# Optimization experiments

Measured on AMD Instinct MI355X. Metric: run time of the kernel, lower is better.

## Reference

```python
import jax, jax.numpy as jnp
import numpy as np

NUM_ROUTES = 32 * 6 * 6  # 1152
NUM_CAPS = 10
IN_DIM = 8
OUT_DIM = 16
NUM_ITERS = 3

def _conv(x, w, stride):
    return jax.lax.conv_general_dilated(
        x, w, window_strides=(stride, stride), padding='VALID',
        dimension_numbers=('NCHW', 'OIHW', 'NCHW'))

def _squash(u):
    # squash over last axis, exactly as torch code (no eps)
    sn = (u ** 2).sum(-1, keepdims=True)
    return sn * u / ((1.0 + sn) * jnp.sqrt(sn))

def setup_inputs() -> dict:
    key = jax.random.key(0)
    ks = jax.random.split(key, 10)
    B = 512
    data = jax.random.normal(ks[0], (B, 1, 28, 28), dtype=jnp.float32)
    conv_w = jax.random.normal(ks[1], (256, 1, 9, 9), dtype=jnp.float32) * 0.05
    conv_b = jnp.zeros((256,), dtype=jnp.float32)
    # 8 primary-capsule convs stacked caps-major -> fused conv [8*32,256,9,9]
    pc_w = jax.random.normal(ks[2], (8 * 32, 256, 9, 9), dtype=jnp.float32) * 0.01
    pc_b = jnp.zeros((8 * 32,), dtype=jnp.float32)
    W = jax.random.normal(ks[3], (NUM_ROUTES, NUM_CAPS, OUT_DIM, IN_DIM), dtype=jnp.float32)
    enc_w1 = jax.random.normal(ks[4], (512, OUT_DIM * NUM_CAPS), dtype=jnp.float32) * 0.05
    enc_b1 = jnp.zeros((512,), dtype=jnp.float32)
    enc_w2 = jax.random.normal(ks[5], (9, 512), dtype=jnp.float32) * 0.05
    enc_b2 = jnp.zeros((9,), dtype=jnp.float32)
    return dict(data=data, conv_w=conv_w, conv_b=conv_b, pc_w=pc_w, pc_b=pc_b,
                W=W, enc_w1=enc_w1, enc_b1=enc_b1, enc_w2=enc_w2, enc_b2=enc_b2)

def reference(data, conv_w, conv_b, pc_w, pc_b, W, enc_w1, enc_b1, enc_w2, enc_b2):
    B = data.shape[0]
    # ConvLayer: conv + relu -> [B,256,20,20]
    x = jax.nn.relu(_conv(data, conv_w, 1) + conv_b[None, :, None, None])
    # PrimaryCaps: 8 stride-2 convs (fused, caps-major channels) -> [B,256,6,6]
    u = _conv(x, pc_w, 2) + pc_b[None, :, None, None]
    # torch: stack(dim=1) then view(B, num_routes, -1) == reshape caps-major flat
    u = u.reshape(B, NUM_ROUTES, IN_DIM)
    u = _squash(u)  # [B,R,8]
    # WaferCaps: u_hat[b,r,c,o] = sum_i W[r,c,o,i] * u[b,r,i]
    u_hat = jnp.einsum('rcoi,bri->brco', W, u)  # [B,R,C,O]
    b_ij = jnp.zeros((NUM_ROUTES, NUM_CAPS), dtype=u_hat.dtype)
    v = None
    for it in range(NUM_ITERS):
        c_ij = jax.nn.softmax(b_ij, axis=0)  # softmax over routes (dim=1 in torch)
        s = jnp.einsum('rc,brco->bco', c_ij, u_hat)  # [B,C,O]
        # original squashes [B,1,C,O,1] over last (size-1) dim -> elementwise
        s2 = s ** 2
        v = s2 * s / ((1.0 + s2) * jnp.sqrt(s2))  # = s*|s|/(1+s^2)
        if it < NUM_ITERS - 1:
            a = jnp.einsum('brco,bco->brc', u_hat, v)  # [B,R,C]
            b_ij = b_ij + a.mean(axis=0)
    # Encoder: flatten [B,C,O] row-major -> [B,160]
    flat = v.reshape(B, NUM_CAPS * OUT_DIM)
    h = jax.nn.relu(flat @ enc_w1.T + enc_b1)  # dropout is identity at eval
    out = jax.nn.sigmoid(h @ enc_w2.T + enc_b2)
    return out
```

## Files before the change

### kernel.cpp

```cpp
#include <hip/hip_runtime.h>
#include <hip/hip_bf16.h>
#include <stdint.h>


typedef __bf16 bf16_t;
typedef __bf16 bf16x4 __attribute__((ext_vector_type(4)));
typedef __bf16 bf16x8 __attribute__((ext_vector_type(8)));
typedef float f32x4 __attribute__((ext_vector_type(4)));
typedef int i32x4 __attribute__((ext_vector_type(4)));
typedef int i32x8 __attribute__((ext_vector_type(8)));

__device__ __forceinline__ void gload_lds16(const void* g, void* l) {
    __builtin_amdgcn_global_load_lds((const __attribute__((address_space(1))) void*)g,
                                     (__attribute__((address_space(3))) void*)l, 16, 0, 0);
}

#define MEMBAR() asm volatile("" ::: "memory")

__device__ __forceinline__ uint8_t fp8b(float v) {
    return (uint8_t)(__builtin_amdgcn_cvt_pk_fp8_f32(v, 0.f, 0, false) & 0xFF);
}

__global__ __launch_bounds__(256) void k_prep(const float* __restrict__ w1,
                                              const float* __restrict__ cw,
                                              const float* __restrict__ pcw,
                                              float* __restrict__ w1t,
                                              bf16_t* __restrict__ Bc1,
                                              float* __restrict__ bij,
                                              uint8_t* __restrict__ w2t8) {
    __shared__ uint16_t tmp16[10368];
    int blk = blockIdx.x, tid = threadIdx.x;
    if (blk < 45) {
        int i = blk * 256 + tid;
        if (i < 11520) bij[i] = 0.f;
    } else if (blk < 365) {
        int i = (blk - 45) * 256 + tid;
        int j = i / 160, k = i % 160;
        w1t[k * 512 + j] = w1[i];
    } else if (blk < 469) {
        int i = (blk - 365) * 256 + tid;
        if (i < 26624) {
            int oc = i / 104, k = i % 104;
            Bc1[i] = (k < 81) ? (bf16_t)cw[oc * 81 + k] : (bf16_t)0.f;
        }
    } else {
        int oc = blk - 469;
        const float* src = pcw + (size_t)oc * 20736;
        for (int q2 = tid; q2 < 10368; q2 += 256) {
            float a = src[q2 * 2] * 64.f;
            float b = src[q2 * 2 + 1] * 64.f;
            uint32_t pk = __builtin_amdgcn_cvt_pk_fp8_f32(a, b, 0, false);
            tmp16[q2] = (uint16_t)(pk & 0xFFFF);
        }
        __syncthreads();
        uint32_t* dst = (uint32_t*)(w2t8 + (size_t)oc * 20736);
        for (int w = tid; w < 5184; w += 256) {
            int k = w * 4;
            int t = k >> 8, ic0 = k & 255;
            uint32_t r = 0;
#pragma unroll
            for (int j = 0; j < 4; ++j) {
                int s = (ic0 + j) * 81 + t;
                uint32_t b = (tmp16[s >> 1] >> ((s & 1) * 8)) & 0xFF;
                r |= b << (8 * j);
            }
            dst[w] = r;
        }
    }
}

__global__ __launch_bounds__(512) void k_c1gemm(const float* __restrict__ data,
                                                const bf16_t* __restrict__ Bc1,
                                                const float* __restrict__ cb,
                                                uint8_t* __restrict__ xt8) {
    __shared__ __align__(16) bf16_t As[128 * 104];
    __shared__ __align__(16) bf16_t Bs[256 * 104];
    int tid = threadIdx.x, lane = tid & 63, wave = tid >> 6;
    int wm = wave >> 2, wn = wave & 3;
    for (int i = tid; i < 3328; i += 512) {
        int byte = i * 16;
        int r = byte / 208;
        int c16 = (byte - r * 208) >> 4;
        gload_lds16(Bc1 + r * 104 + c16 * 8, (char*)Bs + byte);
    }
    int mr = wm * 64 + (lane & 15);
    int nr = wn * 64 + (lane & 15);
    float bias[4];
#pragma unroll
    for (int nj = 0; nj < 4; ++nj) bias[nj] = cb[nr + nj * 16];

    int m0 = blockIdx.x * 128;
    for (int z = tid; z < 128 * 23; z += 512) {
        int r = z / 23, k = 81 + z - (z / 23) * 23;
        As[r * 104 + k] = (bf16_t)0.f;
    }
    for (int pr = tid; pr < 1152; pr += 512) {
        int r = pr / 9, kh = pr - (pr / 9) * 9;
        int m = m0 + r;
        int b = m / 400, pos = m - b * 400;
        int oh = pos / 20, ow = pos - oh * 20;
        const float* src = data + (size_t)b * 784 + (oh + kh) * 28 + ow;
        bf16_t* dst = &As[r * 104 + kh * 9];
#pragma unroll
        for (int j = 0; j < 9; ++j) dst[j] = (bf16_t)src[j];
    }
    asm volatile("s_waitcnt vmcnt(0)" ::: "memory");
    __syncthreads();
    f32x4 acc[4][4];
#pragma unroll
    for (int mi = 0; mi < 4; ++mi)
#pragma unroll
        for (int nj = 0; nj < 4; ++nj) acc[mi][nj] = (f32x4){0.f, 0.f, 0.f, 0.f};
#pragma unroll
    for (int kk = 0; kk < 3; ++kk) {
        int ch = (kk * 4 + (lane >> 4)) * 8;
        bf16x8 af[4], bfr[4];
#pragma unroll
        for (int i = 0; i < 4; ++i) af[i] = *(const bf16x8*)&As[(mr + i * 16) * 104 + ch];
#pragma unroll
        for (int j = 0; j < 4; ++j) bfr[j] = *(const bf16x8*)&Bs[(nr + j * 16) * 104 + ch];
#pragma unroll
        for (int mi = 0; mi < 4; ++mi)
#pragma unroll
            for (int nj = 0; nj < 4; ++nj)
                acc[mi][nj] = __builtin_amdgcn_mfma_f32_16x16x32_bf16(af[mi], bfr[nj], acc[mi][nj], 0, 0, 0);
    }
    int mbase = m0 + wm * 64 + (lane >> 4) * 4;
#pragma unroll
    for (int mi = 0; mi < 4; ++mi)
#pragma unroll
        for (int nj = 0; nj < 4; ++nj)
#pragma unroll
            for (int j = 0; j < 4; ++j)
                xt8[(size_t)(mbase + mi * 16 + j) * 256 + nr + nj * 16] =
                    fp8b(fmaxf(acc[mi][nj][j] + bias[nj], 0.f));
}

__global__ __launch_bounds__(256) void k_pcgemm(const uint8_t* __restrict__ xt8,
                                                const uint8_t* __restrict__ w2t8,
                                                bf16_t* __restrict__ parts) {
    __shared__ __align__(16) uint8_t As[128 * 128];
    __shared__ __align__(16) uint8_t Bs[64 * 128];
    int bid = blockIdx.x;
    int mt = bid % 144;
    int nt = (bid / 144) & 3;
    int ks = bid / 576;
    int m0 = mt * 128, n0 = nt * 64;
    int tid = threadIdx.x, lane = tid & 63, wave = tid >> 6;

    int csrc = (tid & 7) ^ ((tid >> 3) & 7);
    int arow[4];
#pragma unroll
    for (int p = 0; p < 4; ++p) {
        int m = m0 + p * 32 + (tid >> 3);
        int bb = m / 36, pos = m % 36;
        int oh = pos / 6, ow = pos % 6;
        arow[p] = ((bb * 20 + oh * 2) * 20 + ow * 2) * 256;
    }
    const uint8_t* bbase = w2t8 + (size_t)(n0 + (tid >> 3)) * 20736 + csrc * 16;

    f32x4 acc[4][2];
#pragma unroll
    for (int mi = 0; mi < 4; ++mi)
#pragma unroll
        for (int ni = 0; ni < 2; ++ni) acc[mi][ni] = (f32x4){0.f, 0.f, 0.f, 0.f};

    int g0 = ks * 81;
    int mr = (wave >> 1) * 64 + (lane & 15);
    int nr = (wave & 1) * 32 + (lane & 15);
    int rx = lane & 7;
    int c0 = (2 * (lane >> 4)) ^ rx;
    int c1 = (2 * (lane >> 4) + 1) ^ rx;

    for (int it = 0; it < 81; ++it) {
        int g = g0 + it;
        int t = g >> 1, icb = g & 1;
        int kh = t / 9, kw = t - (t / 9) * 9;
        int aoff = (kh * 20 + kw) * 256 + icb * 128 + csrc * 16;
#pragma unroll
        for (int p = 0; p < 4; ++p)
            gload_lds16(xt8 + arow[p] + aoff, &As[p * 4096 + tid * 16]);
#pragma unroll
        for (int p = 0; p < 2; ++p)
            gload_lds16(bbase + (size_t)p * 32 * 20736 + (size_t)g * 128, &Bs[p * 4096 + tid * 16]);
        __syncthreads();
        i32x8 af[4], bfr[2];
#pragma unroll
        for (int i = 0; i < 4; ++i) {
            i32x4 lo = *(const i32x4*)&As[(mr + i * 16) * 128 + c0 * 16];
            i32x4 hi = *(const i32x4*)&As[(mr + i * 16) * 128 + c1 * 16];
            af[i][0] = lo[0]; af[i][1] = lo[1]; af[i][2] = lo[2]; af[i][3] = lo[3];
            af[i][4] = hi[0]; af[i][5] = hi[1]; af[i][6] = hi[2]; af[i][7] = hi[3];
        }
#pragma unroll
        for (int i = 0; i < 2; ++i) {
            i32x4 lo = *(const i32x4*)&Bs[(nr + i * 16) * 128 + c0 * 16];
            i32x4 hi = *(const i32x4*)&Bs[(nr + i * 16) * 128 + c1 * 16];
            bfr[i][0] = lo[0]; bfr[i][1] = lo[1]; bfr[i][2] = lo[2]; bfr[i][3] = lo[3];
            bfr[i][4] = hi[0]; bfr[i][5] = hi[1]; bfr[i][6] = hi[2]; bfr[i][7] = hi[3];
        }
#pragma unroll
        for (int mi = 0; mi < 4; ++mi)
#pragma unroll
            for (int ni = 0; ni < 2; ++ni)
                acc[mi][ni] = __builtin_amdgcn_mfma_scale_f32_16x16x128_f8f6f4(
                    af[mi], bfr[ni], acc[mi][ni], 0, 0, 0, 0x7F7F7F7F, 0, 0x79797979);
        __syncthreads();
    }

    bf16_t* out = parts + (size_t)ks * 4718592;
    int mbase = m0 + (wave >> 1) * 64 + (lane >> 4) * 4;
    int nbase = n0 + (wave & 1) * 32 + (lane & 15);
#pragma unroll
    for (int mi = 0; mi < 4; ++mi)
#pragma unroll
        for (int ni = 0; ni < 2; ++ni)
#pragma unroll
            for (int j = 0; j < 4; ++j)
                out[(size_t)(mbase + mi * 16 + j) * 256 + nbase + ni * 16] = (bf16_t)acc[mi][ni][j];
}

__global__ __launch_bounds__(256) void k_squash(const bf16_t* __restrict__ parts,
                                                const float* __restrict__ pcb,
                                                bf16_t* __restrict__ ub) {
    __shared__ float s[36 * 257];
    int b = blockIdx.x, tid = threadIdx.x;
    for (int i = tid; i < 9216; i += 256) {
        float a = pcb[i & 255];
#pragma unroll
        for (int p = 0; p < 2; ++p) a += (float)parts[(size_t)p * 4718592 + (size_t)b * 9216 + i];
        s[(i >> 8) * 257 + (i & 255)] = a;
    }
    __syncthreads();
    for (int r = tid; r < 1152; r += 256) {
        int flat0 = r * 8;
        float val[8], sn = 0.f;
#pragma unroll
        for (int e = 0; e < 8; ++e) {
            int f = flat0 + e;
            float x = s[(f % 36) * 257 + f / 36];
            val[e] = x;
            sn += x * x;
        }
        float scale = sn / ((1.f + sn) * sqrtf(sn));
        bf16x8 vv;
#pragma unroll
        for (int e = 0; e < 8; ++e) vv[e] = (bf16_t)(val[e] * scale);
        *(bf16x8*)&ub[(size_t)b * 9216 + flat0] = vv;
    }
}

__global__ __launch_bounds__(256) void k_uT(const bf16_t* __restrict__ ub, bf16_t* __restrict__ uT) {
    __shared__ bf16_t t[64 * 66];
    int kt = blockIdx.x % 144, bt = blockIdx.x / 144;
    int k0 = kt * 64, b0 = bt * 64;
    int tid = threadIdx.x;
    int c8 = tid & 7;
#pragma unroll
    for (int p = 0; p < 2; ++p) {
        int r = p * 32 + (tid >> 3);
        bf16x8 vv = *(const bf16x8*)&ub[(size_t)(b0 + r) * 9216 + k0 + c8 * 8];
        uint32_t u4[4];
        *(bf16x8*)u4 = vv;
#pragma unroll
        for (int j2 = 0; j2 < 4; ++j2)
            *(uint32_t*)&t[r * 66 + c8 * 8 + j2 * 2] = u4[j2];
    }
    __syncthreads();
#pragma unroll
    for (int p = 0; p < 2; ++p) {
        int kp = p * 32 + (tid >> 3);
        bf16x8 vv;
#pragma unroll
        for (int j = 0; j < 8; ++j) vv[j] = t[(c8 * 8 + j) * 66 + kp];
        *(bf16x8*)&uT[(size_t)(k0 + kp) * 512 + b0 + c8 * 8] = vv;
    }
}

__global__ void k_cij(const float* __restrict__ bij, float* __restrict__ cij) {
    __shared__ float red[256];
    int c = blockIdx.x, tid = threadIdx.x;
    float mx = -1e30f;
    for (int r = tid; r < 1152; r += 256) mx = fmaxf(mx, bij[r * 10 + c]);
    red[tid] = mx; __syncthreads();
    for (int s = 128; s > 0; s >>= 1) { if (tid < s) red[tid] = fmaxf(red[tid], red[tid + s]); __syncthreads(); }
    float MX = red[0]; __syncthreads();
    float sm = 0.f;
    for (int r = tid; r < 1152; r += 256) sm += expf(bij[r * 10 + c] - MX);
    red[tid] = sm; __syncthreads();
    for (int s = 128; s > 0; s >>= 1) { if (tid < s) red[tid] += red[tid + s]; __syncthreads(); }
    float inv = 1.f / red[0];
    for (int r = tid; r < 1152; r += 256) cij[r * 10 + c] = expf(bij[r * 10 + c] - MX) * inv;
}

__global__ void k_fold(const float* __restrict__ cij, const float* __restrict__ W,
                       bf16_t* __restrict__ cw2T) {
    int idx = blockIdx.x * 256 + threadIdx.x;
    int co = idx / 9216, k = idx % 9216;
    int r = k >> 3, i = k & 7;
    int c = co >> 4, o = co & 15;
    cw2T[idx] = (bf16_t)(cij[r * 10 + c] * W[((size_t)(r * 10 + c) * 16 + o) * 8 + i]);
}

__global__ void k_fold0(const float* __restrict__ W, bf16_t* __restrict__ cw2T) {
    int idx = blockIdx.x * 256 + threadIdx.x;
    int co = idx / 9216, k = idx % 9216;
    int r = k >> 3, i = k & 7;
    int c = co >> 4, o = co & 15;
    cw2T[idx] = (bf16_t)(W[((size_t)(r * 10 + c) * 16 + o) * 8 + i] * (1.0f / 1152.0f));
}

__global__ __launch_bounds__(256) void k_rgemm(const bf16_t* __restrict__ A,
                                               const bf16_t* __restrict__ B,
                                               bf16_t* __restrict__ Cp,
                                               int Kfull, int steps, int mtiles) {
    __shared__ __align__(16) bf16_t As[64 * 64];
    __shared__ __align__(16) bf16_t Bs[160 * 64];
    int bid = blockIdx.x;
    int mt = bid % mtiles, ks = bid / mtiles;
    int m0 = mt * 64;
    int k0 = ks * steps * 64;
    int tid = threadIdx.x, lane = tid & 63, wave = tid >> 6;
    int srow = tid >> 3;
    int csrc = (tid & 7) ^ (srow & 7);
    const bf16_t* asrc[2];
    const bf16_t* bsrc[5];
#pragma unroll
    for (int p = 0; p < 2; ++p)
        asrc[p] = A + (size_t)(m0 + p * 32 + srow) * Kfull + k0 + csrc * 8;
#pragma unroll
    for (int p = 0; p < 5; ++p)
        bsrc[p] = B + (size_t)(p * 32 + srow) * Kfull + k0 + csrc * 8;

    f32x4 acc[2][5];
#pragma unroll
    for (int mi = 0; mi < 2; ++mi)
#pragma unroll
        for (int nj = 0; nj < 5; ++nj) acc[mi][nj] = (f32x4){0.f, 0.f, 0.f, 0.f};

    int mr = (wave >> 1) * 32 + (lane & 15);
    int nr = (wave & 1) * 80 + (lane & 15);
    int rx = lane & 7;

    for (int it = 0; it < steps; ++it) {
#pragma unroll
        for (int p = 0; p < 2; ++p) gload_lds16(asrc[p] + it * 64, As + p * 2048 + tid * 8);
#pragma unroll
        for (int p = 0; p < 5; ++p) gload_lds16(bsrc[p] + it * 64, Bs + p * 2048 + tid * 8);
        __syncthreads();
#pragma unroll
        for (int kk = 0; kk < 2; ++kk) {
            int ch = ((kk * 4 + (lane >> 4)) ^ rx) * 8;
            bf16x8 af[2], bfr[5];
#pragma unroll
            for (int i = 0; i < 2; ++i) af[i] = *(const bf16x8*)&As[(mr + i * 16) * 64 + ch];
#pragma unroll
            for (int j = 0; j < 5; ++j) bfr[j] = *(const bf16x8*)&Bs[(nr + j * 16) * 64 + ch];
#pragma unroll
            for (int mi = 0; mi < 2; ++mi)
#pragma unroll
                for (int nj = 0; nj < 5; ++nj)
                    acc[mi][nj] = __builtin_amdgcn_mfma_f32_16x16x32_bf16(af[mi], bfr[nj], acc[mi][nj], 0, 0, 0);
        }
        __syncthreads();
    }

    bf16_t* out = Cp + (size_t)ks * ((size_t)mtiles * 64 * 160);
    int mbase = m0 + (wave >> 1) * 32 + (lane >> 4) * 4;
    int nbase = (wave & 1) * 80 + (lane & 15);
#pragma unroll
    for (int mi = 0; mi < 2; ++mi)
#pragma unroll
        for (int nj = 0; nj < 5; ++nj)
#pragma unroll
            for (int j = 0; j < 4; ++j)
                out[(size_t)(mbase + mi * 16 + j) * 160 + nbase + nj * 16] = (bf16_t)acc[mi][nj][j];
}

__global__ void k_vcomp(const bf16_t* __restrict__ sp, float* __restrict__ v,
                        bf16_t* __restrict__ vT) {
    int idx = blockIdx.x * 256 + threadIdx.x;
    float s = 0.f;
    for (int p = 0; p < 72; ++p) s += (float)sp[(size_t)p * 81920 + idx];
    float val = s * fabsf(s) / (1.f + s * s);
    v[idx] = val;
    int b = idx / 160, co = idx % 160;
    vT[(size_t)co * 512 + b] = (bf16_t)val;
}

__global__ __launch_bounds__(256) void k_ggemm2(const bf16_t* __restrict__ uT,
                                                const bf16_t* __restrict__ vT,
                                                const float* __restrict__ W,
                                                float* __restrict__ bij) {
    __shared__ __align__(16) bf16_t As[64 * 64];
    __shared__ __align__(16) bf16_t Bs[160 * 64];
    __shared__ float Gl[64 * 161];
    int mt = blockIdx.x;
    int m0 = mt * 64;
    int tid = threadIdx.x, lane = tid & 63, wave = tid >> 6;
    int srow = tid >> 3;
    int csrc = (tid & 7) ^ (srow & 7);
    const bf16_t* asrc[2];
    const bf16_t* bsrc[5];
#pragma unroll
    for (int p = 0; p < 2; ++p)
        asrc[p] = uT + (size_t)(m0 + p * 32 + srow) * 512 + csrc * 8;
#pragma unroll
    for (int p = 0; p < 5; ++p)
        bsrc[p] = vT + (size_t)(p * 32 + srow) * 512 + csrc * 8;

    f32x4 acc[2][5];
#pragma unroll
    for (int mi = 0; mi < 2; ++mi)
#pragma unroll
        for (int nj = 0; nj < 5; ++nj) acc[mi][nj] = (f32x4){0.f, 0.f, 0.f, 0.f};

    int mr = (wave >> 1) * 32 + (lane & 15);
    int nr = (wave & 1) * 80 + (lane & 15);
    int rx = lane & 7;

    for (int it = 0; it < 8; ++it) {
#pragma unroll
        for (int p = 0; p < 2; ++p) gload_lds16(asrc[p] + it * 64, As + p * 2048 + tid * 8);
#pragma unroll
        for (int p = 0; p < 5; ++p) gload_lds16(bsrc[p] + it * 64, Bs + p * 2048 + tid * 8);
        __syncthreads();
#pragma unroll
        for (int kk = 0; kk < 2; ++kk) {
            int ch = ((kk * 4 + (lane >> 4)) ^ rx) * 8;
            bf16x8 af[2], bfr[5];
#pragma unroll
            for (int i = 0; i < 2; ++i) af[i] = *(const bf16x8*)&As[(mr + i * 16) * 64 + ch];
#pragma unroll
            for (int j = 0; j < 5; ++j) bfr[j] = *(const bf16x8*)&Bs[(nr + j * 16) * 64 + ch];
#pragma unroll
            for (int mi = 0; mi < 2; ++mi)
#pragma unroll
                for (int nj = 0; nj < 5; ++nj)
                    acc[mi][nj] = __builtin_amdgcn_mfma_f32_16x16x32_bf16(af[mi], bfr[nj], acc[mi][nj], 0, 0, 0);
        }
        __syncthreads();
    }

    int mbl = (wave >> 1) * 32 + (lane >> 4) * 4;
    int nbase = (wave & 1) * 80 + (lane & 15);
#pragma unroll
    for (int mi = 0; mi < 2; ++mi)
#pragma unroll
        for (int nj = 0; nj < 5; ++nj)
#pragma unroll
            for (int j = 0; j < 4; ++j)
                Gl[(mbl + mi * 16 + j) * 161 + nbase + nj * 16] = acc[mi][nj][j] * (1.0f / 512.0f);
    __syncthreads();
    if (tid < 80) {
        int rl = tid / 10, c = tid % 10;
        int r = mt * 8 + rl;
        const float* wbase = W + (size_t)(r * 10 + c) * 128;
        float s = 0.f;
#pragma unroll
        for (int o = 0; o < 16; ++o)
#pragma unroll
            for (int i = 0; i < 8; ++i)
                s += wbase[o * 8 + i] * Gl[(rl * 8 + i) * 161 + c * 16 + o];
        bij[r * 10 + c] += s;
    }
}

__global__ __launch_bounds__(256) void k_enc(const float* __restrict__ v,
                                             const float* __restrict__ w1t,
                                             const float* __restrict__ b1,
                                             const float* __restrict__ w2,
                                             const float* __restrict__ b2,
                                             float* __restrict__ out) {
    __shared__ float fl[4 * 160];
    __shared__ float h[4 * 512];
    int b0 = blockIdx.x * 4, tid = threadIdx.x;
    for (int i = tid; i < 640; i += 256) fl[i] = v[(size_t)b0 * 160 + i];
    __syncthreads();
    for (int j = tid; j < 512; j += 256) {
        float bb = b1[j];
        float a0 = bb, a1 = bb, a2 = bb, a3 = bb;
        for (int k = 0; k < 160; ++k) {
            float w = w1t[k * 512 + j];
            a0 += fl[k] * w;
            a1 += fl[160 + k] * w;
            a2 += fl[320 + k] * w;
            a3 += fl[480 + k] * w;
        }
        h[j] = fmaxf(a0, 0.f);
        h[512 + j] = fmaxf(a1, 0.f);
        h[1024 + j] = fmaxf(a2, 0.f);
        h[1536 + j] = fmaxf(a3, 0.f);
    }
    __syncthreads();
    int wave = tid >> 6, lane = tid & 63;
    int q = wave;
    for (int j = 0; j < 9; ++j) {
        float p = 0.f;
#pragma unroll
        for (int l = lane; l < 512; l += 64) p += h[q * 512 + l] * w2[j * 512 + l];
#pragma unroll
        for (int off = 32; off > 0; off >>= 1) p += __shfl_down(p, off, 64);
        if (lane == 0) out[(b0 + q) * 9 + j] = 1.f / (1.f + expf(-(p + b2[j])));
    }
}

extern "C" void kernel_launch(void* const* d_in, const int* in_sizes, int n_in,
                              void* d_out, int out_size, void* d_ws, size_t ws_size,
                              hipStream_t stream) {
    const float* data   = (const float*)d_in[0];
    const float* conv_w = (const float*)d_in[1];
    const float* conv_b = (const float*)d_in[2];
    const float* pc_w   = (const float*)d_in[3];
    const float* pc_b   = (const float*)d_in[4];
    const float* W      = (const float*)d_in[5];
    const float* enc_w1 = (const float*)d_in[6];
    const float* enc_b1 = (const float*)d_in[7];
    const float* enc_w2 = (const float*)d_in[8];
    const float* enc_b2 = (const float*)d_in[9];

    char* ws = (char*)d_ws;
    uint8_t* xt8   = (uint8_t*)(ws + 0);
    uint8_t* w2t8  = (uint8_t*)(ws + 52428800);
    bf16_t*  parts = (bf16_t*)(ws + 57737216);
    bf16_t*  uT    = (bf16_t*)(ws + 76611584);
    bf16_t*  cw2T  = (bf16_t*)(ws + 86048768);
    bf16_t*  sp    = (bf16_t*)(ws + 88997888);
    bf16_t*  ub    = (bf16_t*)(ws + 100794368);
    float*   v     = (float*)(ws + 110231552);
    bf16_t*  vT    = (bf16_t*)(ws + 110559232);
    float*   w1t   = (float*)(ws + 110723072);
    float*   bij   = (float*)(ws + 111050752);
    float*   cij   = (float*)(ws + 111096832);
    bf16_t*  Bc1   = (bf16_t*)(ws + 111142912);
    float*   outp  = (float*)d_out;

    hipLaunchKernelGGL(k_prep, dim3(725), dim3(256), 0, stream, enc_w1, conv_w, pc_w, w1t, Bc1, bij, w2t8);
    hipLaunchKernelGGL(k_c1gemm, dim3(1600), dim3(512), 0, stream, data, Bc1, conv_b, xt8);
    hipLaunchKernelGGL(k_pcgemm, dim3(1152), dim3(256), 0, stream, xt8, w2t8, parts);
    hipLaunchKernelGGL(k_squash, dim3(512), dim3(256), 0, stream, parts, pc_b, ub);
    hipLaunchKernelGGL(k_uT, dim3(1152), dim3(256), 0, stream, ub, uT);
    for (int it = 0; it < 3; ++it) {
        if (it == 0) {
            hipLaunchKernelGGL(k_fold0, dim3(5760), dim3(256), 0, stream, W, cw2T);
        } else {
            hipLaunchKernelGGL(k_cij, dim3(10), dim3(256), 0, stream, bij, cij);
            hipLaunchKernelGGL(k_fold, dim3(5760), dim3(256), 0, stream, cij, W, cw2T);
        }
        hipLaunchKernelGGL(k_rgemm, dim3(576), dim3(256), 0, stream, ub, cw2T, sp, 9216, 2, 8);
        hipLaunchKernelGGL(k_vcomp, dim3(320), dim3(256), 0, stream, sp, v, vT);
        if (it < 2) {
            hipLaunchKernelGGL(k_ggemm2, dim3(144), dim3(256), 0, stream, uT, vT, W, bij);
        }
    }
    hipLaunchKernelGGL(k_enc, dim3(128), dim3(256), 0, stream, v, w1t, enc_b1, enc_w2, enc_b2, outp);
}
```

Baseline: 293.4 us.

## Fuse coupling-weight fold into routing GEMM and widen primary-caps GEMM tile

The separate fold kernels that built the scaled bf16 weight matrix cw2T are removed. The routing GEMM now reads W and cij directly, multiplies them and converts to bf16 while staging its B tile into LDS. Iteration 0 relies on k_cij over the zero-initialized bij, which gives a uniform 1/1152. The routing GEMM uses twice the K steps per block, so there are half as many partial sums to reduce in k_vcomp. The primary-caps fp8 GEMM tile is widened from 128x64 to 128x128, which halves the grid and doubles MFMA work per A-tile load, at the cost of more registers and LDS per block.

```diff
diff --git a/kernel.cpp b/kernel.cpp
--- a/kernel.cpp
+++ b/kernel.cpp
@@ -140,12 +140,12 @@
                                                 const uint8_t* __restrict__ w2t8,
                                                 bf16_t* __restrict__ parts) {
     __shared__ __align__(16) uint8_t As[128 * 128];
-    __shared__ __align__(16) uint8_t Bs[64 * 128];
+    __shared__ __align__(16) uint8_t Bs[128 * 128];
     int bid = blockIdx.x;
     int mt = bid % 144;
-    int nt = (bid / 144) & 3;
-    int ks = bid / 576;
-    int m0 = mt * 128, n0 = nt * 64;
+    int nt = (bid / 144) & 1;
+    int ks = bid / 288;
+    int m0 = mt * 128, n0 = nt * 128;
     int tid = threadIdx.x, lane = tid & 63, wave = tid >> 6;
 
     int csrc = (tid & 7) ^ ((tid >> 3) & 7);
@@ -159,15 +159,15 @@
     }
     const uint8_t* bbase = w2t8 + (size_t)(n0 + (tid >> 3)) * 20736 + csrc * 16;
 
-    f32x4 acc[4][2];
+    f32x4 acc[4][4];
 #pragma unroll
     for (int mi = 0; mi < 4; ++mi)
 #pragma unroll
-        for (int ni = 0; ni < 2; ++ni) acc[mi][ni] = (f32x4){0.f, 0.f, 0.f, 0.f};
+        for (int ni = 0; ni < 4; ++ni) acc[mi][ni] = (f32x4){0.f, 0.f, 0.f, 0.f};
 
     int g0 = ks * 81;
     int mr = (wave >> 1) * 64 + (lane & 15);
-    int nr = (wave & 1) * 32 + (lane & 15);
+    int nr = (wave & 1) * 64 + (lane & 15);
     int rx = lane & 7;
     int c0 = (2 * (lane >> 4)) ^ rx;
     int c1 = (2 * (lane >> 4) + 1) ^ rx;
@@ -178,13 +178,12 @@
         int kh = t / 9, kw = t - (t / 9) * 9;
         int aoff = (kh * 20 + kw) * 256 + icb * 128 + csrc * 16;
 #pragma unroll
-        for (int p = 0; p < 4; ++p)
+        for (int p = 0; p < 4; ++p) {
             gload_lds16(xt8 + arow[p] + aoff, &As[p * 4096 + tid * 16]);
-#pragma unroll
-        for (int p = 0; p < 2; ++p)
             gload_lds16(bbase + (size_t)p * 32 * 20736 + (size_t)g * 128, &Bs[p * 4096 + tid * 16]);
-        __syncthreads();
-        i32x8 af[4], bfr[2];
+        }
+        __syncthreads();
+        i32x8 af[4], bfr[4];
 #pragma unroll
         for (int i = 0; i < 4; ++i) {
             i32x4 lo = *(const i32x4*)&As[(mr + i * 16) * 128 + c0 * 16];
@@ -193,7 +192,7 @@
             af[i][4] = hi[0]; af[i][5] = hi[1]; af[i][6] = hi[2]; af[i][7] = hi[3];
         }
 #pragma unroll
-        for (int i = 0; i < 2; ++i) {
+        for (int i = 0; i < 4; ++i) {
             i32x4 lo = *(const i32x4*)&Bs[(nr + i * 16) * 128 + c0 * 16];
             i32x4 hi = *(const i32x4*)&Bs[(nr + i * 16) * 128 + c1 * 16];
             bfr[i][0] = lo[0]; bfr[i][1] = lo[1]; bfr[i][2] = lo[2]; bfr[i][3] = lo[3];
@@ -202,7 +201,7 @@
 #pragma unroll
         for (int mi = 0; mi < 4; ++mi)
 #pragma unroll
-            for (int ni = 0; ni < 2; ++ni)
+            for (int ni = 0; ni < 4; ++ni)
                 acc[mi][ni] = __builtin_amdgcn_mfma_scale_f32_16x16x128_f8f6f4(
                     af[mi], bfr[ni], acc[mi][ni], 0, 0, 0, 0x7F7F7F7F, 0, 0x79797979);
         __syncthreads();
@@ -210,11 +209,11 @@
 
     bf16_t* out = parts + (size_t)ks * 4718592;
     int mbase = m0 + (wave >> 1) * 64 + (lane >> 4) * 4;
-    int nbase = n0 + (wave & 1) * 32 + (lane & 15);
+    int nbase = n0 + (wave & 1) * 64 + (lane & 15);
 #pragma unroll
     for (int mi = 0; mi < 4; ++mi)
 #pragma unroll
-        for (int ni = 0; ni < 2; ++ni)
+        for (int ni = 0; ni < 4; ++ni)
 #pragma unroll
             for (int j = 0; j < 4; ++j)
                 out[(size_t)(mbase + mi * 16 + j) * 256 + nbase + ni * 16] = (bf16_t)acc[mi][ni][j];
@@ -293,25 +292,9 @@
     for (int r = tid; r < 1152; r += 256) cij[r * 10 + c] = expf(bij[r * 10 + c] - MX) * inv;
 }
 
-__global__ void k_fold(const float* __restrict__ cij, const float* __restrict__ W,
-                       bf16_t* __restrict__ cw2T) {
-    int idx = blockIdx.x * 256 + threadIdx.x;
-    int co = idx / 9216, k = idx % 9216;
-    int r = k >> 3, i = k & 7;
-    int c = co >> 4, o = co & 15;
-    cw2T[idx] = (bf16_t)(cij[r * 10 + c] * W[((size_t)(r * 10 + c) * 16 + o) * 8 + i]);
-}
-
-__global__ void k_fold0(const float* __restrict__ W, bf16_t* __restrict__ cw2T) {
-    int idx = blockIdx.x * 256 + threadIdx.x;
-    int co = idx / 9216, k = idx % 9216;
-    int r = k >> 3, i = k & 7;
-    int c = co >> 4, o = co & 15;
-    cw2T[idx] = (bf16_t)(W[((size_t)(r * 10 + c) * 16 + o) * 8 + i] * (1.0f / 1152.0f));
-}
-
 __global__ __launch_bounds__(256) void k_rgemm(const bf16_t* __restrict__ A,
-                                               const bf16_t* __restrict__ B,
+                                               const float* __restrict__ W,
+                                               const float* __restrict__ cij,
                                                bf16_t* __restrict__ Cp,
                                                int Kfull, int steps, int mtiles) {
     __shared__ __align__(16) bf16_t As[64 * 64];
@@ -324,13 +307,16 @@
     int srow = tid >> 3;
     int csrc = (tid & 7) ^ (srow & 7);
     const bf16_t* asrc[2];
-    const bf16_t* bsrc[5];
 #pragma unroll
     for (int p = 0; p < 2; ++p)
         asrc[p] = A + (size_t)(m0 + p * 32 + srow) * Kfull + k0 + csrc * 8;
-#pragma unroll
-    for (int p = 0; p < 5; ++p)
-        bsrc[p] = B + (size_t)(p * 32 + srow) * Kfull + k0 + csrc * 8;
+    int co_c[5], co_o[5];
+#pragma unroll
+    for (int p = 0; p < 5; ++p) {
+        int co = p * 32 + srow;
+        co_c[p] = co >> 4;
+        co_o[p] = co & 15;
+    }
 
     f32x4 acc[2][5];
 #pragma unroll
@@ -345,8 +331,21 @@
     for (int it = 0; it < steps; ++it) {
 #pragma unroll
         for (int p = 0; p < 2; ++p) gload_lds16(asrc[p] + it * 64, As + p * 2048 + tid * 8);
-#pragma unroll
-        for (int p = 0; p < 5; ++p) gload_lds16(bsrc[p] + it * 64, Bs + p * 2048 + tid * 8);
+        int kr = (k0 >> 3) + it * 8 + csrc;
+#pragma unroll
+        for (int p = 0; p < 5; ++p) {
+            int rc = kr * 10 + co_c[p];
+            float cv = cij[rc];
+            const float* wp = W + ((size_t)rc << 7) + co_o[p] * 8;
+            f32x4 w0 = *(const f32x4*)wp;
+            f32x4 w1 = *(const f32x4*)(wp + 4);
+            bf16x8 bb;
+            bb[0] = (bf16_t)(cv * w0.x); bb[1] = (bf16_t)(cv * w0.y);
+            bb[2] = (bf16_t)(cv * w0.z); bb[3] = (bf16_t)(cv * w0.w);
+            bb[4] = (bf16_t)(cv * w1.x); bb[5] = (bf16_t)(cv * w1.y);
+            bb[6] = (bf16_t)(cv * w1.z); bb[7] = (bf16_t)(cv * w1.w);
+            *(bf16x8*)&Bs[p * 2048 + tid * 8] = bb;
+        }
         __syncthreads();
 #pragma unroll
         for (int kk = 0; kk < 2; ++kk) {
@@ -381,7 +380,8 @@
                         bf16_t* __restrict__ vT) {
     int idx = blockIdx.x * 256 + threadIdx.x;
     float s = 0.f;
-    for (int p = 0; p < 72; ++p) s += (float)sp[(size_t)p * 81920 + idx];
+#pragma unroll
+    for (int p = 0; p < 36; ++p) s += (float)sp[(size_t)p * 81920 + idx];
     float val = s * fabsf(s) / (1.f + s * s);
     v[idx] = val;
     int b = idx / 160, co = idx % 160;
@@ -524,30 +524,24 @@
     uint8_t* w2t8  = (uint8_t*)(ws + 52428800);
     bf16_t*  parts = (bf16_t*)(ws + 57737216);
     bf16_t*  uT    = (bf16_t*)(ws + 76611584);
-    bf16_t*  cw2T  = (bf16_t*)(ws + 86048768);
-    bf16_t*  sp    = (bf16_t*)(ws + 88997888);
-    bf16_t*  ub    = (bf16_t*)(ws + 100794368);
-    float*   v     = (float*)(ws + 110231552);
-    bf16_t*  vT    = (bf16_t*)(ws + 110559232);
-    float*   w1t   = (float*)(ws + 110723072);
-    float*   bij   = (float*)(ws + 111050752);
-    float*   cij   = (float*)(ws + 111096832);
-    bf16_t*  Bc1   = (bf16_t*)(ws + 111142912);
+    bf16_t*  sp    = (bf16_t*)(ws + 86048768);
+    bf16_t*  ub    = (bf16_t*)(ws + 91947008);
+    float*   v     = (float*)(ws + 101384192);
+    bf16_t*  vT    = (bf16_t*)(ws + 101711872);
+    float*   w1t   = (float*)(ws + 101875712);
+    float*   bij   = (float*)(ws + 102203392);
+    float*   cij   = (float*)(ws + 102249472);
+    bf16_t*  Bc1   = (bf16_t*)(ws + 102295552);
     float*   outp  = (float*)d_out;
 
     hipLaunchKernelGGL(k_prep, dim3(725), dim3(256), 0, stream, enc_w1, conv_w, pc_w, w1t, Bc1, bij, w2t8);
     hipLaunchKernelGGL(k_c1gemm, dim3(1600), dim3(512), 0, stream, data, Bc1, conv_b, xt8);
-    hipLaunchKernelGGL(k_pcgemm, dim3(1152), dim3(256), 0, stream, xt8, w2t8, parts);
+    hipLaunchKernelGGL(k_pcgemm, dim3(576), dim3(256), 0, stream, xt8, w2t8, parts);
     hipLaunchKernelGGL(k_squash, dim3(512), dim3(256), 0, stream, parts, pc_b, ub);
     hipLaunchKernelGGL(k_uT, dim3(1152), dim3(256), 0, stream, ub, uT);
     for (int it = 0; it < 3; ++it) {
-        if (it == 0) {
-            hipLaunchKernelGGL(k_fold0, dim3(5760), dim3(256), 0, stream, W, cw2T);
-        } else {
-            hipLaunchKernelGGL(k_cij, dim3(10), dim3(256), 0, stream, bij, cij);
-            hipLaunchKernelGGL(k_fold, dim3(5760), dim3(256), 0, stream, cij, W, cw2T);
-        }
-        hipLaunchKernelGGL(k_rgemm, dim3(576), dim3(256), 0, stream, ub, cw2T, sp, 9216, 2, 8);
+        hipLaunchKernelGGL(k_cij, dim3(10), dim3(256), 0, stream, bij, cij);
+        hipLaunchKernelGGL(k_rgemm, dim3(288), dim3(256), 0, stream, ub, W, cij, sp, 9216, 4, 8);
         hipLaunchKernelGGL(k_vcomp, dim3(320), dim3(256), 0, stream, sp, v, vT);
         if (it < 2) {
             hipLaunchKernelGGL(k_ggemm2, dim3(144), dim3(256), 0, stream, uT, vT, W, bij);
```

New measurement: 291.1 us. About the same (-0.8%).
